# Performance work log

Hardware: AMD Instinct MI355X
Metric: run time of the kernel (lower is better)

The kernel has to match this reference:

```python
import jax, jax.numpy as jnp
import numpy as np

N_POP = 10000.0   # total population N
DT = 0.01         # integration step
EPS = 1e-6        # clamp floor, matches torch .clamp(min=1e-06)
B = 32768         # number of Monte-Carlo trajectories
NUM_STEPS = 1000  # int(T / dt) with T=10, dt=0.01


def setup_inputs() -> dict:
    key = jax.random.key(0)
    k_dw, = jax.random.split(key, 1)
    beta = jnp.array([0.3], dtype=jnp.float32)
    sigma = jnp.array([0.2], dtype=jnp.float32)
    gamma = jnp.array([0.1], dtype=jnp.float32)
    S0 = jnp.full((B,), 9990.0, dtype=jnp.float32)
    E0 = jnp.zeros((B,), dtype=jnp.float32)
    I0 = jnp.full((B,), 10.0, dtype=jnp.float32)
    R0 = jnp.zeros((B,), dtype=jnp.float32)
    # Brownian increments before sqrt(dt) scaling; shared across batch as in the
    # original (torch.randn(4, 1) per step regardless of batch size).
    dW = jax.random.normal(k_dw, (NUM_STEPS, 4), dtype=jnp.float32)
    return {"beta": beta, "sigma": sigma, "gamma": gamma,
            "S0": S0, "E0": E0, "I0": I0, "R0": R0, "dW": dW}


def reference(beta, sigma, gamma, S0, E0, I0, R0, dW):
    b, sg, gm = beta[0], sigma[0], gamma[0]
    dWs = dW * jnp.sqrt(jnp.float32(DT))  # [num_steps, 4], scaled increments

    def step(carry, dw):
        S, E, I, R = carry
        S = jnp.maximum(S, EPS)
        E = jnp.maximum(E, EPS)
        I = jnp.maximum(I, EPS)
        R = jnp.maximum(R, EPS)
        inf_rate = b * S * I / N_POP          # beta*S*I/N
        exp_rate = sg * E                     # sigma*E
        rec_rate = gm * I                     # gamma*I
        # drift
        dS = -inf_rate * DT
        dE = (inf_rate - exp_rate) * DT
        dI = (exp_rate - rec_rate) * DT
        dR = rec_rate * DT
        # diffusion (g @ dW with the sparse structure of g_S..g_R)
        n_inf = jnp.sqrt(inf_rate)
        n_exp = jnp.sqrt(exp_rate)
        n_rec = jnp.sqrt(rec_rate)
        S_n = S + dS - n_inf * dw[0]
        E_n = E + dE + n_inf * dw[0] - n_exp * dw[1]
        I_n = I + dI + n_exp * dw[1] - n_rec * dw[2]
        R_n = R + dR + n_rec * dw[2]
        return (S_n, E_n, I_n, R_n), jnp.stack([S_n, E_n, I_n, R_n])  # [4, B]

    _, traj = jax.lax.scan(step, (S0, E0, I0, R0), dWs)
    return traj  # [num_steps, 4, B]: S/E/I/R trajectories
```

## Files before the change

kernel.cpp:

```cpp
#include <hip/hip_runtime.h>


constexpr int   B_TRAJ  = 32768;
constexpr int   NSTEPS  = 1000;
constexpr float DT      = 0.01f;
constexpr float EPS     = 1e-6f;
constexpr float INV_N   = 1.0f / 10000.0f;

__global__ __launch_bounds__(64) void seir_sde_kernel(
    const float* __restrict__ beta,
    const float* __restrict__ sigma,
    const float* __restrict__ gamma,
    const float* __restrict__ S0,
    const float* __restrict__ E0,
    const float* __restrict__ I0,
    const float* __restrict__ R0,
    const float4* __restrict__ dW,
    float* __restrict__ out)
{
    __shared__ float4 wbuf[NSTEPS];
    const float sdt = 0.1f;
    for (int i = threadIdx.x; i < NSTEPS; i += 64) {
        const float4 w = dW[i];
        wbuf[i] = make_float4(w.x * sdt, w.y * sdt, w.z * sdt, 0.0f);
    }

    const int b = blockIdx.x * 64 + threadIdx.x;
    const float btn = beta[0] * INV_N;
    const float sg  = sigma[0];
    const float gm  = gamma[0];

    float S = S0[b];
    float E = E0[b];
    float I = I0[b];
    float R = R0[b];

    float* o = out + b;

    __syncthreads();

    static_assert(NSTEPS % 20 == 0, "unroll tail not handled");
    #pragma unroll 20
    for (int s = 0; s < NSTEPS; ++s) {
        const float4 w = wbuf[s];

        S = fmaxf(S, EPS);
        E = fmaxf(E, EPS);
        I = fmaxf(I, EPS);
        R = fmaxf(R, EPS);

        const float inf_rate = btn * S * I;
        const float exp_rate = sg * E;
        const float rec_rate = gm * I;

        const float n_inf = __builtin_amdgcn_sqrtf(inf_rate);
        const float n_exp = __builtin_amdgcn_sqrtf(exp_rate);
        const float n_rec = __builtin_amdgcn_sqrtf(rec_rate);

        const float a_inf = n_inf * w.x;
        const float a_exp = n_exp * w.y;
        const float a_rec = n_rec * w.z;

        const float Sn = S - inf_rate * DT              - a_inf;
        const float En = E + (inf_rate - exp_rate) * DT + a_inf - a_exp;
        const float In = I + (exp_rate - rec_rate) * DT + a_exp - a_rec;
        const float Rn = R + rec_rate * DT              + a_rec;

        o[0 * B_TRAJ] = Sn;
        o[1 * B_TRAJ] = En;
        o[2 * B_TRAJ] = In;
        o[3 * B_TRAJ] = Rn;
        o += 4 * B_TRAJ;

        S = Sn; E = En; I = In; R = Rn;
    }
}

extern "C" void kernel_launch(void* const* d_in, const int* in_sizes, int n_in,
                              void* d_out, int out_size, void* d_ws, size_t ws_size,
                              hipStream_t stream) {
    const float*  beta  = (const float*)d_in[0];
    const float*  sigma = (const float*)d_in[1];
    const float*  gamma = (const float*)d_in[2];
    const float*  S0    = (const float*)d_in[3];
    const float*  E0    = (const float*)d_in[4];
    const float*  I0    = (const float*)d_in[5];
    const float*  R0    = (const float*)d_in[6];
    const float4* dW    = (const float4*)d_in[7];
    float* out = (float*)d_out;

    seir_sde_kernel<<<B_TRAJ / 64, 64, 0, stream>>>(
        beta, sigma, gamma, S0, E0, I0, R0, dW, out);
}
```

Baseline: 109.9 us.

## Warp-specialize SDE: compute wave fills LDS ring, store wave writes float4

Each block gains a second wavefront. Wave 0 integrates 20 steps at a time into a double-buffered LDS ring, while wave 1 drains the previous chunk to global memory with 16-byte float4 stores. This separates the serial recurrence from the output stores and widens the store transactions. In exchange it adds a block barrier every 20 steps, extra LDS traffic, and double the threads per block.

```diff
diff --git a/kernel.cpp b/kernel.cpp
--- a/kernel.cpp
+++ b/kernel.cpp
@@ -3,11 +3,13 @@
 
 constexpr int   B_TRAJ  = 32768;
 constexpr int   NSTEPS  = 1000;
+constexpr int   K       = 20;
+constexpr int   NC      = NSTEPS / K;
 constexpr float DT      = 0.01f;
 constexpr float EPS     = 1e-6f;
 constexpr float INV_N   = 1.0f / 10000.0f;
 
-__global__ __launch_bounds__(64) void seir_sde_kernel(
+__global__ __launch_bounds__(128) void seir_sde_kernel(
     const float* __restrict__ beta,
     const float* __restrict__ sigma,
     const float* __restrict__ gamma,
@@ -19,60 +21,94 @@
     float* __restrict__ out)
 {
     __shared__ float4 wbuf[NSTEPS];
+    __shared__ float  ring[2][K][4][64];
+
     const float sdt = 0.1f;
-    for (int i = threadIdx.x; i < NSTEPS; i += 64) {
+    for (int i = threadIdx.x; i < NSTEPS; i += 128) {
         const float4 w = dW[i];
         wbuf[i] = make_float4(w.x * sdt, w.y * sdt, w.z * sdt, 0.0f);
     }
 
-    const int b = blockIdx.x * 64 + threadIdx.x;
-    const float btn = beta[0] * INV_N;
-    const float sg  = sigma[0];
-    const float gm  = gamma[0];
+    const int lane = threadIdx.x & 63;
+    const int wid  = threadIdx.x >> 6;
 
-    float S = S0[b];
-    float E = E0[b];
-    float I = I0[b];
-    float R = R0[b];
+    float S = 0.f, E = 0.f, I = 0.f, R = 0.f, btn = 0.f, sg = 0.f, gm = 0.f;
+    if (wid == 0) {
+        const int b = blockIdx.x * 64 + lane;
+        S = S0[b]; E = E0[b]; I = I0[b]; R = R0[b];
+        btn = beta[0] * INV_N; sg = sigma[0]; gm = gamma[0];
+    }
 
-    float* o = out + b;
+    float* const obase = out + blockIdx.x * 64
+                             + (lane >> 4) * B_TRAJ + (lane & 15) * 4;
 
     __syncthreads();
 
-    static_assert(NSTEPS % 20 == 0, "unroll tail not handled");
-    #pragma unroll 20
-    for (int s = 0; s < NSTEPS; ++s) {
-        const float4 w = wbuf[s];
+    if (wid == 0) {
+        #pragma unroll 5
+        for (int k = 0; k < K; ++k) {
+            const float4 w = wbuf[k];
+            S = fmaxf(S, EPS); E = fmaxf(E, EPS);
+            I = fmaxf(I, EPS); R = fmaxf(R, EPS);
+            const float inf = btn * S * I;
+            const float ex  = sg * E;
+            const float rc  = gm * I;
+            const float ni = __builtin_amdgcn_sqrtf(inf);
+            const float ne = __builtin_amdgcn_sqrtf(ex);
+            const float nr = __builtin_amdgcn_sqrtf(rc);
+            const float ai = ni * w.x, ae = ne * w.y, ar = nr * w.z;
+            const float Sn = S - inf * DT             - ai;
+            const float En = E + (inf - ex) * DT + ai - ae;
+            const float In = I + (ex - rc) * DT  + ae - ar;
+            const float Rn = R + rc * DT              + ar;
+            ring[0][k][0][lane] = Sn;
+            ring[0][k][1][lane] = En;
+            ring[0][k][2][lane] = In;
+            ring[0][k][3][lane] = Rn;
+            S = Sn; E = En; I = In; R = Rn;
+        }
+    }
+    __syncthreads();
 
-        S = fmaxf(S, EPS);
-        E = fmaxf(E, EPS);
-        I = fmaxf(I, EPS);
-        R = fmaxf(R, EPS);
-
-        const float inf_rate = btn * S * I;
-        const float exp_rate = sg * E;
-        const float rec_rate = gm * I;
-
-        const float n_inf = __builtin_amdgcn_sqrtf(inf_rate);
-        const float n_exp = __builtin_amdgcn_sqrtf(exp_rate);
-        const float n_rec = __builtin_amdgcn_sqrtf(rec_rate);
-
-        const float a_inf = n_inf * w.x;
-        const float a_exp = n_exp * w.y;
-        const float a_rec = n_rec * w.z;
-
-        const float Sn = S - inf_rate * DT              - a_inf;
-        const float En = E + (inf_rate - exp_rate) * DT + a_inf - a_exp;
-        const float In = I + (exp_rate - rec_rate) * DT + a_exp - a_rec;
-        const float Rn = R + rec_rate * DT              + a_rec;
-
-        o[0 * B_TRAJ] = Sn;
-        o[1 * B_TRAJ] = En;
-        o[2 * B_TRAJ] = In;
-        o[3 * B_TRAJ] = Rn;
-        o += 4 * B_TRAJ;
-
-        S = Sn; E = En; I = In; R = Rn;
+    for (int c = 0; c < NC; ++c) {
+        if (wid == 0) {
+            if (c + 1 < NC) {
+                const int s0 = (c + 1) * K;
+                float (*rw)[4][64] = ring[(c + 1) & 1];
+                #pragma unroll 5
+                for (int k = 0; k < K; ++k) {
+                    const float4 w = wbuf[s0 + k];
+                    S = fmaxf(S, EPS); E = fmaxf(E, EPS);
+                    I = fmaxf(I, EPS); R = fmaxf(R, EPS);
+                    const float inf = btn * S * I;
+                    const float ex  = sg * E;
+                    const float rc  = gm * I;
+                    const float ni = __builtin_amdgcn_sqrtf(inf);
+                    const float ne = __builtin_amdgcn_sqrtf(ex);
+                    const float nr = __builtin_amdgcn_sqrtf(rc);
+                    const float ai = ni * w.x, ae = ne * w.y, ar = nr * w.z;
+                    const float Sn = S - inf * DT             - ai;
+                    const float En = E + (inf - ex) * DT + ai - ae;
+                    const float In = I + (ex - rc) * DT  + ae - ar;
+                    const float Rn = R + rc * DT              + ar;
+                    rw[k][0][lane] = Sn;
+                    rw[k][1][lane] = En;
+                    rw[k][2][lane] = In;
+                    rw[k][3][lane] = Rn;
+                    S = Sn; E = En; I = In; R = Rn;
+                }
+            }
+        } else {
+            const float4* rd = (const float4*)&ring[c & 1][0][0][0];
+            float* o = obase + (size_t)(c * K) * (4 * B_TRAJ);
+            #pragma unroll
+            for (int k = 0; k < K; ++k) {
+                const float4 v = rd[k * 64 + lane];
+                *(float4*)o = v;
+                o += 4 * B_TRAJ;
+            }
+        }
+        __syncthreads();
     }
 }
 
@@ -89,6 +125,6 @@
     const float4* dW    = (const float4*)d_in[7];
     float* out = (float*)d_out;
 
-    seir_sde_kernel<<<B_TRAJ / 64, 64, 0, stream>>>(
+    seir_sde_kernel<<<B_TRAJ / 64, 128, 0, stream>>>(
         beta, sigma, gamma, S0, E0, I0, R0, dW, out);
 }
```

New measurement: 97.21 us. 1.13x faster.
